# Kernel tuning notes

Measured on AMD Instinct MI355X. Metric: run time of the kernel, lower is better.

## Reference

```python
import jax, jax.numpy as jnp
import numpy as np

B, D, C, P = 1024, 768, 150, 64  # batch, in_feats, num_labels, proj2 dim
POS_M, NEG_M = 0.7, 1.4


def setup_inputs() -> dict:
    key = jax.random.key(0)
    ks = jax.random.split(key, 8)
    return {
        "x": jax.random.normal(ks[0], (B, D), jnp.float32),
        "lb": jax.random.randint(ks[1], (B,), 0, C + 1),
        "mem": jax.random.normal(ks[2], (C, D), jnp.float32),
        "fc_w": jax.random.normal(ks[3], (2 * D, 2 * D), jnp.float32) * 0.02,
        "fc_b": jnp.zeros((2 * D,), jnp.float32),
        "p1_w": jax.random.normal(ks[4], (1, 2 * D), jnp.float32) * 0.02,
        "p1_b": jnp.zeros((1,), jnp.float32),
        "p2_w": jax.random.normal(ks[5], (P, 2 * D), jnp.float32) * 0.02,
        "p2_b": jnp.zeros((P,), jnp.float32),
    }


def reference(x, lb, mem, fc_w, fc_b, p1_w, p1_b, p2_w, p2_b):
    d = x.shape[1]
    # cat([a, b], 1) @ fc_w.T == a @ Wx.T + b @ Wm.T  (exact split of the linear)
    Wx, Wm = fc_w[:, :d], fc_w[:, d:]
    xh = x @ Wx.T + fc_b                                # [B, 2D]

    # --- get_logit ---
    seen_h = jax.nn.relu(xh[:, None, :] + mem @ Wm.T)   # [B, C, 2D]
    seen = jnp.einsum('bce,e->bc', seen_h, p1_w[0]) + p1_b[0]   # [B, C]
    uh = jax.nn.relu(xh)                                # cat([x, zeros]) path
    unseen = uh @ p1_w.T + p1_b                         # [B, 1]
    logits = jnp.concatenate([seen, unseen], axis=1)    # [B, C+1]

    # --- masked log-softmax losses (pos_adapte) ---
    labels = jax.nn.one_hot(lb, C + 1, dtype=jnp.float32)
    th = jnp.zeros_like(labels).at[:, -1].set(1.0)
    labels = labels.at[:, -1].set(0.0)
    p_mask = labels + th
    n_mask = 1.0 - labels
    BIG = 1e30
    loss1 = -(jax.nn.log_softmax(logits - (1.0 - p_mask) * BIG, -1) * labels).sum(1)
    loss2 = -(jax.nn.log_softmax(logits - (1.0 - n_mask) * BIG, -1) * th).sum(1)
    loss_cls = (loss1 + loss2).mean()

    # --- metric loss on unseen embedding ---
    u = uh @ p2_w.T + p2_b                              # [B, 64]
    u = u / jnp.maximum(jnp.linalg.norm(u, axis=1, keepdims=True), 1e-12)
    sq_n = (u * u).sum(1)
    sq = sq_n[:, None] + sq_n[None, :] - 2.0 * (u @ u.T)
    err = sq <= 0.0
    dist = jnp.sqrt(jnp.clip(sq, 1e-16, None)) * (~err).astype(u.dtype)
    same = lb[:, None] == lb[None, :]
    eye = jnp.eye(dist.shape[0], dtype=bool)
    pos = (same & ~eye).astype(dist.dtype)
    neg = (~same).astype(dist.dtype)
    pos_l = (jax.nn.relu(dist - POS_M) * pos).sum() / jnp.maximum(pos.sum(), 1.0)
    neg_l = (jax.nn.relu(NEG_M - dist) * neg).sum() / jnp.maximum(neg.sum(), 1.0)

    return loss_cls + pos_l + neg_l
```

## Files before the change

kernel.cpp:

```cpp
#include <hip/hip_runtime.h>
#include <math.h>

#define B_    1024
#define D_    768
#define C_    150
#define P_    64
#define TWOD  1536
#define NCLS  151
#define CPAD  256

#define ECHUNKS 16
#define ECHUNK  96

#define ASTR  40
#define USTRU 120
#define USTR  72

#define OFF_MH      0
#define OFF_XH      (OFF_MH + (C_ * TWOD) / 2)
#define OFF_PARTIAL (OFF_XH + (B_ * TWOD) / 2)
#define OFF_UHF     (OFF_PARTIAL + ECHUNKS * B_ * CPAD)
#define OFF_SQN     (OFF_UHF + (B_ * P_) / 2)
#define OFF_CLS     (OFF_SQN + B_)
#define OFF_PAIR    (OFF_CLS + B_)
#define OFF_XBF     (OFF_PAIR + 1024)
#define OFF_MEMBF   (OFF_XBF + (B_ * D_) / 2)
#define OFF_WBF     (OFF_MEMBF + (C_ * D_) / 2)
#define OFF_P2H     (OFF_WBF + (TWOD * TWOD) / 2)
#define OFF_P1H     (OFF_P2H + (P_ * TWOD) / 2)

typedef __bf16    bfx8   __attribute__((ext_vector_type(8)));
typedef _Float16  fp16x8 __attribute__((ext_vector_type(8)));
typedef _Float16  h2v    __attribute__((ext_vector_type(2)));
typedef float     f32x4  __attribute__((ext_vector_type(4)));

__device__ inline ushort f2bf(float f) {
    union { float f; unsigned u; } c; c.f = f;
    unsigned r = c.u + 0x7fffu + ((c.u >> 16) & 1u);
    return (ushort)(r >> 16);
}
__device__ inline ushort f2h(float f) {
    _Float16 h = (_Float16)f;
    return __builtin_bit_cast(ushort, h);
}
__device__ inline unsigned addrelu2(unsigned a, unsigned m) {
    h2v s = __builtin_bit_cast(h2v, a) + __builtin_bit_cast(h2v, m);
    h2v z = {(_Float16)0.f, (_Float16)0.f};
    s = __builtin_elementwise_max(s, z);
    return __builtin_bit_cast(unsigned, s);
}
__device__ inline unsigned relu2(unsigned a) {
    h2v s = __builtin_bit_cast(h2v, a);
    h2v z = {(_Float16)0.f, (_Float16)0.f};
    s = __builtin_elementwise_max(s, z);
    return __builtin_bit_cast(unsigned, s);
}
__device__ inline float dot2acc(unsigned a, unsigned b, float c) {
    return __builtin_amdgcn_fdot2(__builtin_bit_cast(h2v, a),
                                  __builtin_bit_cast(h2v, b), c, false);
}

#define X4   (B_ * D_ / 4)
#define MEM4 (C_ * D_ / 4)
#define W4   (TWOD * TWOD / 4)
#define P24  (P_ * TWOD / 4)
#define P14  (TWOD / 4)
#define TOT4 (X4 + MEM4 + W4 + P24 + P14)

__global__ __launch_bounds__(256) void prep_cvt(
    const float* __restrict__ x, const float* __restrict__ mem,
    const float* __restrict__ w, const float* __restrict__ p2w,
    const float* __restrict__ p1w,
    ushort* __restrict__ xb, ushort* __restrict__ memb,
    ushort* __restrict__ wb, ushort* __restrict__ p2h,
    ushort* __restrict__ p1h)
{
    int i = blockIdx.x * 256 + threadIdx.x;
    if (i >= TOT4) return;
    const float* src; ushort* dst; int off; bool bf;
    if (i < X4)                        { src = x;   dst = xb;   off = i; bf = true; }
    else if (i < X4 + MEM4)            { src = mem; dst = memb; off = i - X4; bf = true; }
    else if (i < X4 + MEM4 + W4)       { src = w;   dst = wb;   off = i - X4 - MEM4; bf = true; }
    else if (i < X4 + MEM4 + W4 + P24) { src = p2w; dst = p2h;  off = i - X4 - MEM4 - W4; bf = false; }
    else                               { src = p1w; dst = p1h;  off = i - X4 - MEM4 - W4 - P24; bf = false; }
    float4 v = ((const float4*)src)[off];
    ushort4 o;
    if (bf) { o.x = f2bf(v.x); o.y = f2bf(v.y); o.z = f2bf(v.z); o.w = f2bf(v.w); }
    else    { o.x = f2h(v.x);  o.y = f2h(v.y);  o.z = f2h(v.z);  o.w = f2h(v.w); }
    ((ushort4*)dst)[off] = o;
}

__global__ __launch_bounds__(256) void gemm_all(
    const ushort* __restrict__ xbf, const ushort* __restrict__ membf,
    const ushort* __restrict__ wbf, const float* __restrict__ fc_b,
    ushort* __restrict__ xh, ushort* __restrict__ mh)
{
    __shared__ ushort As[64 * ASTR];
    __shared__ ushort Bs[128 * ASTR];
    const int id = blockIdx.x;
    const int t  = threadIdx.x;

    const ushort* A; ushort* Out; int M, m0, n0, koff; bool xblk;
    if (id < 192) {
        xblk = true;  A = xbf;  Out = xh; M = B_;
        m0 = (id & 15) * 64; n0 = (id >> 4) * 128; koff = 0;
    } else {
        int q = id - 192;
        xblk = false; A = membf; Out = mh; M = C_;
        m0 = (q % 3) * 64; n0 = (q / 3) * 128; koff = D_;
    }

    const int wave = t >> 6, lane = t & 63;
    const int wm = (wave & 1) * 32, wn = (wave >> 1) * 64;
    const int fm = lane & 15, quad = lane >> 4;

    const int row_a = t >> 2, qa = (t & 3) * 8;
    const int ar = min(m0 + row_a, M - 1);
    const ushort* Arow = A + (size_t)ar * D_ + qa;
    const ushort* Brow = wbf + (size_t)(n0 + row_a) * TWOD + koff + qa;

    f32x4 acc[2][4];
#pragma unroll
    for (int j = 0; j < 4; ++j) {
        float bv = xblk ? fc_b[n0 + wn + j * 16 + fm] : 0.f;
#pragma unroll
        for (int i = 0; i < 2; ++i)
            acc[i][j] = (f32x4){bv, bv, bv, bv};
    }

    uint4 pa  = *(const uint4*)(Arow);
    uint4 pb0 = *(const uint4*)(Brow);
    uint4 pb1 = *(const uint4*)(Brow + 64 * TWOD);

    for (int k0 = 0; k0 < D_; k0 += 32) {
        __syncthreads();
        *(uint4*)&As[row_a * ASTR + qa] = pa;
        *(uint4*)&Bs[row_a * ASTR + qa] = pb0;
        *(uint4*)&Bs[(64 + row_a) * ASTR + qa] = pb1;
        __syncthreads();
        if (k0 + 32 < D_) {
            pa  = *(const uint4*)(Arow + k0 + 32);
            pb0 = *(const uint4*)(Brow + k0 + 32);
            pb1 = *(const uint4*)(Brow + 64 * TWOD + k0 + 32);
        }
        bfx8 af[2], bf[4];
#pragma unroll
        for (int i = 0; i < 2; ++i)
            af[i] = *(const bfx8*)&As[(wm + i * 16 + fm) * ASTR + quad * 8];
#pragma unroll
        for (int j = 0; j < 4; ++j)
            bf[j] = *(const bfx8*)&Bs[(wn + j * 16 + fm) * ASTR + quad * 8];
#pragma unroll
        for (int i = 0; i < 2; ++i)
#pragma unroll
            for (int j = 0; j < 4; ++j)
                acc[i][j] = __builtin_amdgcn_mfma_f32_16x16x32_bf16(
                    af[i], bf[j], acc[i][j], 0, 0, 0);
    }

#pragma unroll
    for (int i = 0; i < 2; ++i)
#pragma unroll
        for (int j = 0; j < 4; ++j)
#pragma unroll
            for (int r = 0; r < 4; ++r) {
                int row = m0 + wm + i * 16 + quad * 4 + r;
                int col = n0 + wn + j * 16 + fm;
                if (row < M) Out[(size_t)row * TWOD + col] = f2h(acc[i][j][r]);
            }
}

__global__ __launch_bounds__(256) void fused_tile(
    const ushort* __restrict__ xh, const ushort* __restrict__ mh,
    const ushort* __restrict__ p1h, const ushort* __restrict__ p2h,
    float* __restrict__ partial)
{
    __shared__ __align__(16) char smem[46080];
    const int t  = threadIdx.x;
    const int b0 = blockIdx.x * 128;
    const int z  = blockIdx.z;
    const int e0 = z * ECHUNK;

    if (blockIdx.y == 3) {
        ushort* Au = (ushort*)smem;
        ushort* Wu = (ushort*)(smem + 30720);
        const int wave = t >> 6, lane = t & 63;
        const int fm = lane & 15, quad = lane >> 4;

        {
            const int row = t >> 1, kh = (t & 1) * 48;
            const ushort* src = xh + (size_t)(b0 + row) * TWOD + e0 + kh;
            uint4 v[6];
#pragma unroll
            for (int i = 0; i < 6; ++i) v[i] = *(const uint4*)&src[i * 8];
#pragma unroll
            for (int i = 0; i < 6; ++i) {
                v[i].x = relu2(v[i].x); v[i].y = relu2(v[i].y);
                v[i].z = relu2(v[i].z); v[i].w = relu2(v[i].w);
                *(uint4*)&Au[row * USTRU + kh + i * 8] = v[i];
            }
        }
        {
            const int row = t >> 2, ks = (t & 3) * 24;
            const ushort* pw = p2h + (size_t)row * TWOD + e0 + ks;
#pragma unroll
            for (int i = 0; i < 3; ++i)
                *(uint4*)&Wu[row * USTRU + ks + i * 8] = *(const uint4*)&pw[i * 8];
        }
        __syncthreads();

        f32x4 uacc[2][4];
#pragma unroll
        for (int i = 0; i < 2; ++i)
#pragma unroll
            for (int j = 0; j < 4; ++j) uacc[i][j] = (f32x4){0.f, 0.f, 0.f, 0.f};
#pragma unroll
        for (int k0 = 0; k0 < ECHUNK; k0 += 32) {
            fp16x8 af[2], bf[4];
#pragma unroll
            for (int i = 0; i < 2; ++i)
                af[i] = *(const fp16x8*)&Au[(wave * 32 + i * 16 + fm) * USTRU + k0 + quad * 8];
#pragma unroll
            for (int j = 0; j < 4; ++j)
                bf[j] = *(const fp16x8*)&Wu[(j * 16 + fm) * USTRU + k0 + quad * 8];
#pragma unroll
            for (int i = 0; i < 2; ++i)
#pragma unroll
                for (int j = 0; j < 4; ++j)
                    uacc[i][j] = __builtin_amdgcn_mfma_f32_16x16x32_f16(
                        af[i], bf[j], uacc[i][j], 0, 0, 0);
        }
#pragma unroll
        for (int i = 0; i < 2; ++i)
#pragma unroll
            for (int j = 0; j < 4; ++j)
#pragma unroll
                for (int r = 0; r < 4; ++r) {
                    int row = b0 + wave * 32 + i * 16 + quad * 4 + r;
                    partial[((size_t)z * B_ + row) * CPAD + 192 + j * 16 + fm] =
                        uacc[i][j][r];
                }
        return;
    }

    unsigned* xT = (unsigned*)smem;
    unsigned* mT = (unsigned*)(smem + 24576);
    unsigned* wT = (unsigned*)(smem + 36864);
    const int c0 = blockIdx.y * 64;
    const int tm = t & 15, tn = t >> 4;

    {
        const int row = t >> 1, ph = (t & 1) * 48;
        const ushort* src = xh + (size_t)(b0 + row) * TWOD + e0 + ph;
        uint4 v[6];
#pragma unroll
        for (int i = 0; i < 6; ++i) v[i] = *(const uint4*)&src[i * 8];
#pragma unroll
        for (int i = 0; i < 6; ++i) {
            const int ep = (t & 1) * 24 + i * 4;
            xT[(ep + 0) * 128 + row] = v[i].x;
            xT[(ep + 1) * 128 + row] = v[i].y;
            xT[(ep + 2) * 128 + row] = v[i].z;
            xT[(ep + 3) * 128 + row] = v[i].w;
        }
    }
    {
        const int col = t & 63, seg = t >> 6;
        const int gc  = c0 + col;
        uint4 v[3];
        if (gc < C_) {
            const ushort* src = mh + (size_t)gc * TWOD + e0 + seg * 24;
#pragma unroll
            for (int i = 0; i < 3; ++i) v[i] = *(const uint4*)&src[i * 8];
        } else {
#pragma unroll
            for (int i = 0; i < 3; ++i) v[i] = make_uint4(0, 0, 0, 0);
        }
#pragma unroll
        for (int i = 0; i < 3; ++i) {
            const int ep = seg * 12 + i * 4;
            mT[(ep + 0) * 64 + col] = v[i].x;
            mT[(ep + 1) * 64 + col] = v[i].y;
            mT[(ep + 2) * 64 + col] = v[i].z;
            mT[(ep + 3) * 64 + col] = v[i].w;
        }
    }
    if (t < 12) {
        uint4 v = *(const uint4*)&p1h[e0 + t * 8];
        wT[t * 4 + 0] = v.x; wT[t * 4 + 1] = v.y;
        wT[t * 4 + 2] = v.z; wT[t * 4 + 3] = v.w;
    }
    __syncthreads();

    float acc[8][4] = {};
#pragma unroll 4
    for (int ep = 0; ep < 48; ++ep) {
        uint4 a0 = *(const uint4*)&xT[ep * 128 + tm * 8];
        uint4 a1 = *(const uint4*)&xT[ep * 128 + tm * 8 + 4];
        uint4 mj = *(const uint4*)&mT[ep * 64 + tn * 4];
        const unsigned wv = wT[ep];
        const unsigned aa[8] = {a0.x, a0.y, a0.z, a0.w, a1.x, a1.y, a1.z, a1.w};
        const unsigned mm[4] = {mj.x, mj.y, mj.z, mj.w};
#pragma unroll
        for (int i = 0; i < 8; ++i)
#pragma unroll
            for (int j = 0; j < 4; ++j)
                acc[i][j] = dot2acc(addrelu2(aa[i], mm[j]), wv, acc[i][j]);
    }

#pragma unroll
    for (int i = 0; i < 8; ++i) {
        const int gb = b0 + tm * 8 + i;
        float4 v = make_float4(acc[i][0], acc[i][1], acc[i][2], acc[i][3]);
        *(float4*)&partial[((size_t)z * B_ + gb) * CPAD + c0 + tn * 4] = v;
    }
}

__global__ __launch_bounds__(256) void reduce_row(
    const float* __restrict__ partial,
    const float* __restrict__ p1b, const float* __restrict__ p2b,
    const int* __restrict__ lb,
    ushort* __restrict__ uhf, float* __restrict__ sqn,
    float* __restrict__ clsbuf)
{
    const int b = blockIdx.x, t = threadIdx.x;
    float v = 0.f;
#pragma unroll
    for (int z = 0; z < ECHUNKS; ++z)
        v += partial[((size_t)z * B_ + b) * CPAD + t];
    if (t < NCLS)       v += p1b[0];
    else if (t >= 192)  v += p2b[t - 192];

    __shared__ float sval[256];
    sval[t] = v;
    __syncthreads();

    if (t < 64) {
        float uv = sval[192 + t];
        float s = uv * uv;
#pragma unroll
        for (int off = 32; off; off >>= 1) s += __shfl_xor(s, off);
        float inv = 1.f / fmaxf(sqrtf(s), 1e-12f);
        uhf[(size_t)b * P_ + t] = f2h(uv * inv);
        if (t == 0) sqn[b] = s * inv * inv;

        const int l = lb[b];
        float mx = -1e30f;
        for (int j = t; j < NCLS; j += 64)
            if (!(j == l && l < C_)) mx = fmaxf(mx, sval[j]);
#pragma unroll
        for (int off = 32; off; off >>= 1) mx = fmaxf(mx, __shfl_xor(mx, off));
        float se = 0.f;
        for (int j = t; j < NCLS; j += 64)
            if (!(j == l && l < C_)) se += expf(sval[j] - mx);
#pragma unroll
        for (int off = 32; off; off >>= 1) se += __shfl_xor(se, off);

        if (t == 0) {
            float l150  = sval[C_];
            float loss2 = mx + logf(se) - l150;
            float loss1 = 0.f;
            if (l < C_) {
                float a  = sval[l];
                float m2 = fmaxf(a, l150);
                loss1 = m2 - a + logf(expf(a - m2) + expf(l150 - m2));
            }
            clsbuf[b] = loss1 + loss2;
        }
    }
}

__global__ __launch_bounds__(256) void pair_loss(
    const ushort* __restrict__ uhf, const float* __restrict__ sqn,
    const int* __restrict__ lb, float* __restrict__ pairpart)
{
    __shared__ ushort ui_s[64 * USTR];
    __shared__ ushort uj_s[64 * USTR];
    __shared__ float sni[64], snj[64];
    __shared__ int   li[64],  lj[64];
    __shared__ float red[4][4];

    const int t  = threadIdx.x;
    const int i0 = blockIdx.x * 64, j0 = blockIdx.y * 64;

    for (int idx = t; idx < 512; idx += 256) {
        int row = idx >> 3, ch = (idx & 7) * 8;
        *(uint4*)&ui_s[row * USTR + ch] =
            *(const uint4*)&uhf[(size_t)(i0 + row) * P_ + ch];
        *(uint4*)&uj_s[row * USTR + ch] =
            *(const uint4*)&uhf[(size_t)(j0 + row) * P_ + ch];
    }
    if (t < 64)       { sni[t] = sqn[i0 + t]; li[t] = lb[i0 + t]; }
    else if (t < 128) { int q = t - 64; snj[q] = sqn[j0 + q]; lj[q] = lb[j0 + q]; }
    __syncthreads();

    const int wave = t >> 6, lane = t & 63;
    const int n = lane & 15, quad = lane >> 4;
    const int iw = wave * 16;

    const fp16x8 af0 = *(const fp16x8*)&ui_s[(iw + n) * USTR + quad * 8];
    const fp16x8 af1 = *(const fp16x8*)&ui_s[(iw + n) * USTR + quad * 8 + 32];

    f32x4 acc[4];
#pragma unroll
    for (int jt = 0; jt < 4; ++jt) {
        const fp16x8 bf0 = *(const fp16x8*)&uj_s[(jt * 16 + n) * USTR + quad * 8];
        const fp16x8 bf1 = *(const fp16x8*)&uj_s[(jt * 16 + n) * USTR + quad * 8 + 32];
        acc[jt] = __builtin_amdgcn_mfma_f32_16x16x32_f16(
            af0, bf0, (f32x4){0.f, 0.f, 0.f, 0.f}, 0, 0, 0);
        acc[jt] = __builtin_amdgcn_mfma_f32_16x16x32_f16(
            af1, bf1, acc[jt], 0, 0, 0);
    }

    float ps = 0.f, pc = 0.f, ns = 0.f, nc = 0.f;
#pragma unroll
    for (int jt = 0; jt < 4; ++jt)
#pragma unroll
        for (int r = 0; r < 4; ++r) {
            const int il = iw + quad * 4 + r;
            const int jl = jt * 16 + n;
            float sq = sni[il] + snj[jl] - 2.f * acc[jt][r];
            float dist = sq > 0.f ? sqrtf(fmaxf(sq, 1e-16f)) : 0.f;
            bool same = (li[il] == lj[jl]);
            if (same) {
                if (i0 + il != j0 + jl) { ps += fmaxf(dist - 0.7f, 0.f); pc += 1.f; }
            } else {
                ns += fmaxf(1.4f - dist, 0.f); nc += 1.f;
            }
        }

#pragma unroll
    for (int off = 32; off; off >>= 1) {
        ps += __shfl_xor(ps, off); pc += __shfl_xor(pc, off);
        ns += __shfl_xor(ns, off); nc += __shfl_xor(nc, off);
    }
    if (lane == 0) { red[0][wave] = ps; red[1][wave] = pc;
                     red[2][wave] = ns; red[3][wave] = nc; }
    __syncthreads();
    if (t == 0) {
        float4 v;
        v.x = red[0][0] + red[0][1] + red[0][2] + red[0][3];
        v.y = red[1][0] + red[1][1] + red[1][2] + red[1][3];
        v.z = red[2][0] + red[2][1] + red[2][2] + red[2][3];
        v.w = red[3][0] + red[3][1] + red[3][2] + red[3][3];
        *(float4*)&pairpart[(size_t)(blockIdx.y * 16 + blockIdx.x) * 4] = v;
    }
}

__global__ __launch_bounds__(256) void finalize(
    const float* __restrict__ clsbuf, const float* __restrict__ pairpart,
    float* __restrict__ out)
{
    __shared__ float red[5][4];
    const int t = threadIdx.x;
    float c = clsbuf[t] + clsbuf[t + 256] + clsbuf[t + 512] + clsbuf[t + 768];
    float4 pp = *(const float4*)&pairpart[(size_t)t * 4];
    float ps = pp.x, pc = pp.y, ns = pp.z, nc = pp.w;
#pragma unroll
    for (int off = 32; off; off >>= 1) {
        c  += __shfl_xor(c, off);
        ps += __shfl_xor(ps, off); pc += __shfl_xor(pc, off);
        ns += __shfl_xor(ns, off); nc += __shfl_xor(nc, off);
    }
    const int wave = t >> 6, lane = t & 63;
    if (lane == 0) { red[0][wave] = c; red[1][wave] = ps; red[2][wave] = pc;
                     red[3][wave] = ns; red[4][wave] = nc; }
    __syncthreads();
    if (t == 0) {
        float C = 0.f, PS = 0.f, PC = 0.f, NS = 0.f, NC = 0.f;
#pragma unroll
        for (int w = 0; w < 4; ++w) {
            C += red[0][w]; PS += red[1][w]; PC += red[2][w];
            NS += red[3][w]; NC += red[4][w];
        }
        out[0] = C / (float)B_ + PS / fmaxf(PC, 1.f) + NS / fmaxf(NC, 1.f);
    }
}

extern "C" void kernel_launch(void* const* d_in, const int* in_sizes, int n_in,
                              void* d_out, int out_size, void* d_ws, size_t ws_size,
                              hipStream_t stream)
{
    const float* x    = (const float*)d_in[0];
    const int*   lb   = (const int*)d_in[1];
    const float* mem  = (const float*)d_in[2];
    const float* fc_w = (const float*)d_in[3];
    const float* fc_b = (const float*)d_in[4];
    const float* p1w  = (const float*)d_in[5];
    const float* p1b  = (const float*)d_in[6];
    const float* p2w  = (const float*)d_in[7];
    const float* p2b  = (const float*)d_in[8];

    float* ws       = (float*)d_ws;
    ushort* mh      = (ushort*)(ws + OFF_MH);
    ushort* xh      = (ushort*)(ws + OFF_XH);
    float* partials = ws + OFF_PARTIAL;
    ushort* uhf     = (ushort*)(ws + OFF_UHF);
    float* sqn      = ws + OFF_SQN;
    float* clsbuf   = ws + OFF_CLS;
    float* pairpart = ws + OFF_PAIR;
    ushort* xbf     = (ushort*)(ws + OFF_XBF);
    ushort* membf   = (ushort*)(ws + OFF_MEMBF);
    ushort* wbf     = (ushort*)(ws + OFF_WBF);
    ushort* p2h     = (ushort*)(ws + OFF_P2H);
    ushort* p1h     = (ushort*)(ws + OFF_P1H);

    prep_cvt<<<(TOT4 + 255) / 256, 256, 0, stream>>>(x, mem, fc_w, p2w, p1w,
                                                     xbf, membf, wbf, p2h, p1h);
    gemm_all<<<228, 256, 0, stream>>>(xbf, membf, wbf, fc_b, xh, mh);
    fused_tile<<<dim3(8, 4, ECHUNKS), 256, 0, stream>>>(xh, mh, p1h, p2h,
                                                        partials);
    reduce_row<<<B_, 256, 0, stream>>>(partials, p1b, p2b, lb, uhf, sqn, clsbuf);
    pair_loss<<<dim3(16, 16), 256, 0, stream>>>(uhf, sqn, lb, pairpart);
    finalize<<<1, 256, 0, stream>>>(clsbuf, pairpart, (float*)d_out);
}
```

Measured before the change: 132.2 us.

## Merge six kernel launches into one cooperative persistent kernel with grid syncs

Replaces the sequence of prep, GEMM, fused tile, row reduce, pair loss and finalize kernels with a single cooperative kernel of 512 blocks. The stages are separated by grid-wide barriers. This removes per-launch overhead and the gaps between dependent kernels. In exchange, each stage is limited to 512 resident blocks, idle blocks wait at every barrier, and grid.sync itself has a cost.

New measurement: 403.9 us. +205.6%, slower.

```diff
diff --git a/kernel.cpp b/kernel.cpp
--- a/kernel.cpp
+++ b/kernel.cpp
@@ -1,5 +1,8 @@
 #include <hip/hip_runtime.h>
+#include <hip/hip_cooperative_groups.h>
 #include <math.h>
+
+namespace cg = cooperative_groups;
 
 #define B_    1024
 #define D_    768
@@ -67,413 +70,424 @@
 #define P14  (TWOD / 4)
 #define TOT4 (X4 + MEM4 + W4 + P24 + P14)
 
-__global__ __launch_bounds__(256) void prep_cvt(
-    const float* __restrict__ x, const float* __restrict__ mem,
-    const float* __restrict__ w, const float* __restrict__ p2w,
-    const float* __restrict__ p1w,
-    ushort* __restrict__ xb, ushort* __restrict__ memb,
-    ushort* __restrict__ wb, ushort* __restrict__ p2h,
-    ushort* __restrict__ p1h)
+#define GRID_ 512
+
+__global__ __launch_bounds__(256, 2) void mega(
+    const float* __restrict__ x, const int* __restrict__ lb,
+    const float* __restrict__ mem, const float* __restrict__ fcw,
+    const float* __restrict__ fcb, const float* __restrict__ p1w,
+    const float* __restrict__ p1b, const float* __restrict__ p2w,
+    const float* __restrict__ p2b, float* __restrict__ ws,
+    float* __restrict__ out)
 {
-    int i = blockIdx.x * 256 + threadIdx.x;
-    if (i >= TOT4) return;
-    const float* src; ushort* dst; int off; bool bf;
-    if (i < X4)                        { src = x;   dst = xb;   off = i; bf = true; }
-    else if (i < X4 + MEM4)            { src = mem; dst = memb; off = i - X4; bf = true; }
-    else if (i < X4 + MEM4 + W4)       { src = w;   dst = wb;   off = i - X4 - MEM4; bf = true; }
-    else if (i < X4 + MEM4 + W4 + P24) { src = p2w; dst = p2h;  off = i - X4 - MEM4 - W4; bf = false; }
-    else                               { src = p1w; dst = p1h;  off = i - X4 - MEM4 - W4 - P24; bf = false; }
-    float4 v = ((const float4*)src)[off];
-    ushort4 o;
-    if (bf) { o.x = f2bf(v.x); o.y = f2bf(v.y); o.z = f2bf(v.z); o.w = f2bf(v.w); }
-    else    { o.x = f2h(v.x);  o.y = f2h(v.y);  o.z = f2h(v.z);  o.w = f2h(v.w); }
-    ((ushort4*)dst)[off] = o;
-}
-
-__global__ __launch_bounds__(256) void gemm_all(
-    const ushort* __restrict__ xbf, const ushort* __restrict__ membf,
-    const ushort* __restrict__ wbf, const float* __restrict__ fc_b,
-    ushort* __restrict__ xh, ushort* __restrict__ mh)
-{
-    __shared__ ushort As[64 * ASTR];
-    __shared__ ushort Bs[128 * ASTR];
+    __shared__ __align__(16) char smem[46080];
+    cg::grid_group grid = cg::this_grid();
     const int id = blockIdx.x;
     const int t  = threadIdx.x;
 
-    const ushort* A; ushort* Out; int M, m0, n0, koff; bool xblk;
-    if (id < 192) {
-        xblk = true;  A = xbf;  Out = xh; M = B_;
-        m0 = (id & 15) * 64; n0 = (id >> 4) * 128; koff = 0;
-    } else {
-        int q = id - 192;
-        xblk = false; A = membf; Out = mh; M = C_;
-        m0 = (q % 3) * 64; n0 = (q / 3) * 128; koff = D_;
+    ushort* mh       = (ushort*)(ws + OFF_MH);
+    ushort* xh       = (ushort*)(ws + OFF_XH);
+    float*  partial  = ws + OFF_PARTIAL;
+    ushort* uhf      = (ushort*)(ws + OFF_UHF);
+    float*  sqn      = ws + OFF_SQN;
+    float*  clsbuf   = ws + OFF_CLS;
+    float*  pairpart = ws + OFF_PAIR;
+    ushort* xbf      = (ushort*)(ws + OFF_XBF);
+    ushort* membf    = (ushort*)(ws + OFF_MEMBF);
+    ushort* wbf      = (ushort*)(ws + OFF_WBF);
+    ushort* p2h      = (ushort*)(ws + OFF_P2H);
+    ushort* p1h      = (ushort*)(ws + OFF_P1H);
+
+    for (int i = id * 256 + t; i < TOT4; i += GRID_ * 256) {
+        const float* src; ushort* dst; int off; bool bf;
+        if (i < X4)                        { src = x;   dst = xbf;   off = i; bf = true; }
+        else if (i < X4 + MEM4)            { src = mem; dst = membf; off = i - X4; bf = true; }
+        else if (i < X4 + MEM4 + W4)       { src = fcw; dst = wbf;   off = i - X4 - MEM4; bf = true; }
+        else if (i < X4 + MEM4 + W4 + P24) { src = p2w; dst = p2h;   off = i - X4 - MEM4 - W4; bf = false; }
+        else                               { src = p1w; dst = p1h;   off = i - X4 - MEM4 - W4 - P24; bf = false; }
+        float4 v = ((const float4*)src)[off];
+        ushort4 o;
+        if (bf) { o.x = f2bf(v.x); o.y = f2bf(v.y); o.z = f2bf(v.z); o.w = f2bf(v.w); }
+        else    { o.x = f2h(v.x);  o.y = f2h(v.y);  o.z = f2h(v.z);  o.w = f2h(v.w); }
+        ((ushort4*)dst)[off] = o;
     }
 
-    const int wave = t >> 6, lane = t & 63;
-    const int wm = (wave & 1) * 32, wn = (wave >> 1) * 64;
-    const int fm = lane & 15, quad = lane >> 4;
-
-    const int row_a = t >> 2, qa = (t & 3) * 8;
-    const int ar = min(m0 + row_a, M - 1);
-    const ushort* Arow = A + (size_t)ar * D_ + qa;
-    const ushort* Brow = wbf + (size_t)(n0 + row_a) * TWOD + koff + qa;
-
-    f32x4 acc[2][4];
-#pragma unroll
-    for (int j = 0; j < 4; ++j) {
-        float bv = xblk ? fc_b[n0 + wn + j * 16 + fm] : 0.f;
+    grid.sync();
+
+    if (id < 228) {
+        ushort* As = (ushort*)smem;
+        ushort* Bs = (ushort*)(smem + 5120);
+
+        const ushort* A; ushort* Out; int M, m0, n0, koff; bool xblk;
+        if (id < 192) {
+            xblk = true;  A = xbf;   Out = xh; M = B_;
+            m0 = (id & 15) * 64; n0 = (id >> 4) * 128; koff = 0;
+        } else {
+            int q = id - 192;
+            xblk = false; A = membf; Out = mh; M = C_;
+            m0 = (q % 3) * 64; n0 = (q / 3) * 128; koff = D_;
+        }
+
+        const int wave = t >> 6, lane = t & 63;
+        const int wm = (wave & 1) * 32, wn = (wave >> 1) * 64;
+        const int fm = lane & 15, quad = lane >> 4;
+
+        const int row_a = t >> 2, qa = (t & 3) * 8;
+        const int ar = min(m0 + row_a, M - 1);
+        const ushort* Arow = A + (size_t)ar * D_ + qa;
+        const ushort* Brow = wbf + (size_t)(n0 + row_a) * TWOD + koff + qa;
+
+        f32x4 acc[2][4];
+#pragma unroll
+        for (int j = 0; j < 4; ++j) {
+            float bv = xblk ? fcb[n0 + wn + j * 16 + fm] : 0.f;
+#pragma unroll
+            for (int i = 0; i < 2; ++i)
+                acc[i][j] = (f32x4){bv, bv, bv, bv};
+        }
+
+        uint4 pa  = *(const uint4*)(Arow);
+        uint4 pb0 = *(const uint4*)(Brow);
+        uint4 pb1 = *(const uint4*)(Brow + 64 * TWOD);
+
+        for (int k0 = 0; k0 < D_; k0 += 32) {
+            __syncthreads();
+            *(uint4*)&As[row_a * ASTR + qa] = pa;
+            *(uint4*)&Bs[row_a * ASTR + qa] = pb0;
+            *(uint4*)&Bs[(64 + row_a) * ASTR + qa] = pb1;
+            __syncthreads();
+            if (k0 + 32 < D_) {
+                pa  = *(const uint4*)(Arow + k0 + 32);
+                pb0 = *(const uint4*)(Brow + k0 + 32);
+                pb1 = *(const uint4*)(Brow + 64 * TWOD + k0 + 32);
+            }
+            bfx8 af[2], bf[4];
+#pragma unroll
+            for (int i = 0; i < 2; ++i)
+                af[i] = *(const bfx8*)&As[(wm + i * 16 + fm) * ASTR + quad * 8];
+#pragma unroll
+            for (int j = 0; j < 4; ++j)
+                bf[j] = *(const bfx8*)&Bs[(wn + j * 16 + fm) * ASTR + quad * 8];
+#pragma unroll
+            for (int i = 0; i < 2; ++i)
+#pragma unroll
+                for (int j = 0; j < 4; ++j)
+                    acc[i][j] = __builtin_amdgcn_mfma_f32_16x16x32_bf16(
+                        af[i], bf[j], acc[i][j], 0, 0, 0);
+        }
+
 #pragma unroll
         for (int i = 0; i < 2; ++i)
-            acc[i][j] = (f32x4){bv, bv, bv, bv};
+#pragma unroll
+            for (int j = 0; j < 4; ++j)
+#pragma unroll
+                for (int r = 0; r < 4; ++r) {
+                    int row = m0 + wm + i * 16 + quad * 4 + r;
+                    int col = n0 + wn + j * 16 + fm;
+                    if (row < M) Out[(size_t)row * TWOD + col] = f2h(acc[i][j][r]);
+                }
     }
 
-    uint4 pa  = *(const uint4*)(Arow);
-    uint4 pb0 = *(const uint4*)(Brow);
-    uint4 pb1 = *(const uint4*)(Brow + 64 * TWOD);
-
-    for (int k0 = 0; k0 < D_; k0 += 32) {
+    grid.sync();
+
+    {
+        const int bx = id & 7, yy = (id >> 3) & 3, z = id >> 5;
+        const int b0 = bx * 128;
+        const int e0 = z * ECHUNK;
+
+        if (yy == 3) {
+            ushort* Au = (ushort*)smem;
+            ushort* Wu = (ushort*)(smem + 30720);
+            const int wave = t >> 6, lane = t & 63;
+            const int fm = lane & 15, quad = lane >> 4;
+
+            {
+                const int row = t >> 1, kh = (t & 1) * 48;
+                const ushort* src = xh + (size_t)(b0 + row) * TWOD + e0 + kh;
+                uint4 v[6];
+#pragma unroll
+                for (int i = 0; i < 6; ++i) v[i] = *(const uint4*)&src[i * 8];
+#pragma unroll
+                for (int i = 0; i < 6; ++i) {
+                    v[i].x = relu2(v[i].x); v[i].y = relu2(v[i].y);
+                    v[i].z = relu2(v[i].z); v[i].w = relu2(v[i].w);
+                    *(uint4*)&Au[row * USTRU + kh + i * 8] = v[i];
+                }
+            }
+            {
+                const int row = t >> 2, ks = (t & 3) * 24;
+                const ushort* pw = p2h + (size_t)row * TWOD + e0 + ks;
+#pragma unroll
+                for (int i = 0; i < 3; ++i)
+                    *(uint4*)&Wu[row * USTRU + ks + i * 8] = *(const uint4*)&pw[i * 8];
+            }
+            __syncthreads();
+
+            f32x4 uacc[2][4];
+#pragma unroll
+            for (int i = 0; i < 2; ++i)
+#pragma unroll
+                for (int j = 0; j < 4; ++j) uacc[i][j] = (f32x4){0.f, 0.f, 0.f, 0.f};
+#pragma unroll
+            for (int k0 = 0; k0 < ECHUNK; k0 += 32) {
+                fp16x8 af[2], bf[4];
+#pragma unroll
+                for (int i = 0; i < 2; ++i)
+                    af[i] = *(const fp16x8*)&Au[(wave * 32 + i * 16 + fm) * USTRU + k0 + quad * 8];
+#pragma unroll
+                for (int j = 0; j < 4; ++j)
+                    bf[j] = *(const fp16x8*)&Wu[(j * 16 + fm) * USTRU + k0 + quad * 8];
+#pragma unroll
+                for (int i = 0; i < 2; ++i)
+#pragma unroll
+                    for (int j = 0; j < 4; ++j)
+                        uacc[i][j] = __builtin_amdgcn_mfma_f32_16x16x32_f16(
+                            af[i], bf[j], uacc[i][j], 0, 0, 0);
+            }
+#pragma unroll
+            for (int i = 0; i < 2; ++i)
+#pragma unroll
+                for (int j = 0; j < 4; ++j)
+#pragma unroll
+                    for (int r = 0; r < 4; ++r) {
+                        int row = b0 + wave * 32 + i * 16 + quad * 4 + r;
+                        partial[((size_t)z * B_ + row) * CPAD + 192 + j * 16 + fm] =
+                            uacc[i][j][r];
+                    }
+        } else {
+            unsigned* xT = (unsigned*)smem;
+            unsigned* mT = (unsigned*)(smem + 24576);
+            unsigned* wT = (unsigned*)(smem + 36864);
+            const int c0 = yy * 64;
+            const int tm = t & 15, tn = t >> 4;
+
+            {
+                const int row = t >> 1, ph = (t & 1) * 48;
+                const ushort* src = xh + (size_t)(b0 + row) * TWOD + e0 + ph;
+                uint4 v[6];
+#pragma unroll
+                for (int i = 0; i < 6; ++i) v[i] = *(const uint4*)&src[i * 8];
+#pragma unroll
+                for (int i = 0; i < 6; ++i) {
+                    const int ep = (t & 1) * 24 + i * 4;
+                    xT[(ep + 0) * 128 + row] = v[i].x;
+                    xT[(ep + 1) * 128 + row] = v[i].y;
+                    xT[(ep + 2) * 128 + row] = v[i].z;
+                    xT[(ep + 3) * 128 + row] = v[i].w;
+                }
+            }
+            {
+                const int col = t & 63, seg = t >> 6;
+                const int gc  = c0 + col;
+                uint4 v[3];
+                if (gc < C_) {
+                    const ushort* src = mh + (size_t)gc * TWOD + e0 + seg * 24;
+#pragma unroll
+                    for (int i = 0; i < 3; ++i) v[i] = *(const uint4*)&src[i * 8];
+                } else {
+#pragma unroll
+                    for (int i = 0; i < 3; ++i) v[i] = make_uint4(0, 0, 0, 0);
+                }
+#pragma unroll
+                for (int i = 0; i < 3; ++i) {
+                    const int ep = seg * 12 + i * 4;
+                    mT[(ep + 0) * 64 + col] = v[i].x;
+                    mT[(ep + 1) * 64 + col] = v[i].y;
+                    mT[(ep + 2) * 64 + col] = v[i].z;
+                    mT[(ep + 3) * 64 + col] = v[i].w;
+                }
+            }
+            if (t < 12) {
+                uint4 v = *(const uint4*)&p1h[e0 + t * 8];
+                wT[t * 4 + 0] = v.x; wT[t * 4 + 1] = v.y;
+                wT[t * 4 + 2] = v.z; wT[t * 4 + 3] = v.w;
+            }
+            __syncthreads();
+
+            float acc[8][4] = {};
+#pragma unroll 4
+            for (int ep = 0; ep < 48; ++ep) {
+                uint4 a0 = *(const uint4*)&xT[ep * 128 + tm * 8];
+                uint4 a1 = *(const uint4*)&xT[ep * 128 + tm * 8 + 4];
+                uint4 mj = *(const uint4*)&mT[ep * 64 + tn * 4];
+                const unsigned wv = wT[ep];
+                const unsigned aa[8] = {a0.x, a0.y, a0.z, a0.w,
+                                        a1.x, a1.y, a1.z, a1.w};
+                const unsigned mm[4] = {mj.x, mj.y, mj.z, mj.w};
+#pragma unroll
+                for (int i = 0; i < 8; ++i)
+#pragma unroll
+                    for (int j = 0; j < 4; ++j)
+                        acc[i][j] = dot2acc(addrelu2(aa[i], mm[j]), wv, acc[i][j]);
+            }
+
+#pragma unroll
+            for (int i = 0; i < 8; ++i) {
+                const int gb = b0 + tm * 8 + i;
+                float4 v = make_float4(acc[i][0], acc[i][1], acc[i][2], acc[i][3]);
+                *(float4*)&partial[((size_t)z * B_ + gb) * CPAD + c0 + tn * 4] = v;
+            }
+        }
+    }
+
+    grid.sync();
+
+    {
+        float* sval = (float*)smem;
+        for (int rr = 0; rr < 2; ++rr) {
+            const int b = id * 2 + rr;
+            float v = 0.f;
+#pragma unroll
+            for (int z = 0; z < ECHUNKS; ++z)
+                v += partial[((size_t)z * B_ + b) * CPAD + t];
+            if (t < NCLS)       v += p1b[0];
+            else if (t >= 192)  v += p2b[t - 192];
+
+            __syncthreads();
+            sval[t] = v;
+            __syncthreads();
+
+            if (t < 64) {
+                float uv = sval[192 + t];
+                float s = uv * uv;
+#pragma unroll
+                for (int off = 32; off; off >>= 1) s += __shfl_xor(s, off);
+                float inv = 1.f / fmaxf(sqrtf(s), 1e-12f);
+                uhf[(size_t)b * P_ + t] = f2h(uv * inv);
+                if (t == 0) sqn[b] = s * inv * inv;
+
+                const int l = lb[b];
+                float mx = -1e30f;
+                for (int j = t; j < NCLS; j += 64)
+                    if (!(j == l && l < C_)) mx = fmaxf(mx, sval[j]);
+#pragma unroll
+                for (int off = 32; off; off >>= 1) mx = fmaxf(mx, __shfl_xor(mx, off));
+                float se = 0.f;
+                for (int j = t; j < NCLS; j += 64)
+                    if (!(j == l && l < C_)) se += expf(sval[j] - mx);
+#pragma unroll
+                for (int off = 32; off; off >>= 1) se += __shfl_xor(se, off);
+
+                if (t == 0) {
+                    float l150  = sval[C_];
+                    float loss2 = mx + logf(se) - l150;
+                    float loss1 = 0.f;
+                    if (l < C_) {
+                        float a  = sval[l];
+                        float m2 = fmaxf(a, l150);
+                        loss1 = m2 - a + logf(expf(a - m2) + expf(l150 - m2));
+                    }
+                    clsbuf[b] = loss1 + loss2;
+                }
+            }
+        }
+    }
+
+    grid.sync();
+
+    if (id < 256) {
+        ushort* ui_s = (ushort*)smem;
+        ushort* uj_s = (ushort*)(smem + 9216);
+        float*  sni  = (float*)(smem + 18432);
+        float*  snj  = (float*)(smem + 18688);
+        int*    li   = (int*)(smem + 18944);
+        int*    lj   = (int*)(smem + 19200);
+        float*  red  = (float*)(smem + 19456);
+
+        const int i0 = (id & 15) * 64, j0 = (id >> 4) * 64;
+
+        for (int idx = t; idx < 512; idx += 256) {
+            int row = idx >> 3, ch = (idx & 7) * 8;
+            *(uint4*)&ui_s[row * USTR + ch] =
+                *(const uint4*)&uhf[(size_t)(i0 + row) * P_ + ch];
+            *(uint4*)&uj_s[row * USTR + ch] =
+                *(const uint4*)&uhf[(size_t)(j0 + row) * P_ + ch];
+        }
+        if (t < 64)       { sni[t] = sqn[i0 + t]; li[t] = lb[i0 + t]; }
+        else if (t < 128) { int q = t - 64; snj[q] = sqn[j0 + q]; lj[q] = lb[j0 + q]; }
         __syncthreads();
-        *(uint4*)&As[row_a * ASTR + qa] = pa;
-        *(uint4*)&Bs[row_a * ASTR + qa] = pb0;
-        *(uint4*)&Bs[(64 + row_a) * ASTR + qa] = pb1;
+
+        const int wave = t >> 6, lane = t & 63;
+        const int n = lane & 15, quad = lane >> 4;
+        const int iw = wave * 16;
+
+        const fp16x8 af0 = *(const fp16x8*)&ui_s[(iw + n) * USTR + quad * 8];
+        const fp16x8 af1 = *(const fp16x8*)&ui_s[(iw + n) * USTR + quad * 8 + 32];
+
+        f32x4 acc[4];
+#pragma unroll
+        for (int jt = 0; jt < 4; ++jt) {
+            const fp16x8 bf0 = *(const fp16x8*)&uj_s[(jt * 16 + n) * USTR + quad * 8];
+            const fp16x8 bf1 = *(const fp16x8*)&uj_s[(jt * 16 + n) * USTR + quad * 8 + 32];
+            acc[jt] = __builtin_amdgcn_mfma_f32_16x16x32_f16(
+                af0, bf0, (f32x4){0.f, 0.f, 0.f, 0.f}, 0, 0, 0);
+            acc[jt] = __builtin_amdgcn_mfma_f32_16x16x32_f16(
+                af1, bf1, acc[jt], 0, 0, 0);
+        }
+
+        float ps = 0.f, pc = 0.f, ns = 0.f, nc = 0.f;
+#pragma unroll
+        for (int jt = 0; jt < 4; ++jt)
+#pragma unroll
+            for (int r = 0; r < 4; ++r) {
+                const int il = iw + quad * 4 + r;
+                const int jl = jt * 16 + n;
+                float sq = sni[il] + snj[jl] - 2.f * acc[jt][r];
+                float dist = sq > 0.f ? sqrtf(fmaxf(sq, 1e-16f)) : 0.f;
+                bool same = (li[il] == lj[jl]);
+                if (same) {
+                    if (i0 + il != j0 + jl) { ps += fmaxf(dist - 0.7f, 0.f); pc += 1.f; }
+                } else {
+                    ns += fmaxf(1.4f - dist, 0.f); nc += 1.f;
+                }
+            }
+
+#pragma unroll
+        for (int off = 32; off; off >>= 1) {
+            ps += __shfl_xor(ps, off); pc += __shfl_xor(pc, off);
+            ns += __shfl_xor(ns, off); nc += __shfl_xor(nc, off);
+        }
+        if (lane == 0) { red[0 * 4 + wave] = ps; red[1 * 4 + wave] = pc;
+                         red[2 * 4 + wave] = ns; red[3 * 4 + wave] = nc; }
         __syncthreads();
-        if (k0 + 32 < D_) {
-            pa  = *(const uint4*)(Arow + k0 + 32);
-            pb0 = *(const uint4*)(Brow + k0 + 32);
-            pb1 = *(const uint4*)(Brow + 64 * TWOD + k0 + 32);
-        }
-        bfx8 af[2], bf[4];
-#pragma unroll
-        for (int i = 0; i < 2; ++i)
-            af[i] = *(const bfx8*)&As[(wm + i * 16 + fm) * ASTR + quad * 8];
-#pragma unroll
-        for (int j = 0; j < 4; ++j)
-            bf[j] = *(const bfx8*)&Bs[(wn + j * 16 + fm) * ASTR + quad * 8];
-#pragma unroll
-        for (int i = 0; i < 2; ++i)
-#pragma unroll
-            for (int j = 0; j < 4; ++j)
-                acc[i][j] = __builtin_amdgcn_mfma_f32_16x16x32_bf16(
-                    af[i], bf[j], acc[i][j], 0, 0, 0);
+        if (t == 0) {
+            float4 v;
+            v.x = red[0] + red[1] + red[2] + red[3];
+            v.y = red[4] + red[5] + red[6] + red[7];
+            v.z = red[8] + red[9] + red[10] + red[11];
+            v.w = red[12] + red[13] + red[14] + red[15];
+            *(float4*)&pairpart[(size_t)id * 4] = v;
+        }
     }
 
-#pragma unroll
-    for (int i = 0; i < 2; ++i)
-#pragma unroll
-        for (int j = 0; j < 4; ++j)
-#pragma unroll
-            for (int r = 0; r < 4; ++r) {
-                int row = m0 + wm + i * 16 + quad * 4 + r;
-                int col = n0 + wn + j * 16 + fm;
-                if (row < M) Out[(size_t)row * TWOD + col] = f2h(acc[i][j][r]);
-            }
-}
-
-__global__ __launch_bounds__(256) void fused_tile(
-    const ushort* __restrict__ xh, const ushort* __restrict__ mh,
-    const ushort* __restrict__ p1h, const ushort* __restrict__ p2h,
-    float* __restrict__ partial)
-{
-    __shared__ __align__(16) char smem[46080];
-    const int t  = threadIdx.x;
-    const int b0 = blockIdx.x * 128;
-    const int z  = blockIdx.z;
-    const int e0 = z * ECHUNK;
-
-    if (blockIdx.y == 3) {
-        ushort* Au = (ushort*)smem;
-        ushort* Wu = (ushort*)(smem + 30720);
+    grid.sync();
+
+    if (id == 0) {
+        float* red = (float*)smem;
+        float c = clsbuf[t] + clsbuf[t + 256] + clsbuf[t + 512] + clsbuf[t + 768];
+        float4 pp = *(const float4*)&pairpart[(size_t)t * 4];
+        float ps = pp.x, pc = pp.y, ns = pp.z, nc = pp.w;
+#pragma unroll
+        for (int off = 32; off; off >>= 1) {
+            c  += __shfl_xor(c, off);
+            ps += __shfl_xor(ps, off); pc += __shfl_xor(pc, off);
+            ns += __shfl_xor(ns, off); nc += __shfl_xor(nc, off);
+        }
         const int wave = t >> 6, lane = t & 63;
-        const int fm = lane & 15, quad = lane >> 4;
-
-        {
-            const int row = t >> 1, kh = (t & 1) * 48;
-            const ushort* src = xh + (size_t)(b0 + row) * TWOD + e0 + kh;
-            uint4 v[6];
-#pragma unroll
-            for (int i = 0; i < 6; ++i) v[i] = *(const uint4*)&src[i * 8];
-#pragma unroll
-            for (int i = 0; i < 6; ++i) {
-                v[i].x = relu2(v[i].x); v[i].y = relu2(v[i].y);
-                v[i].z = relu2(v[i].z); v[i].w = relu2(v[i].w);
-                *(uint4*)&Au[row * USTRU + kh + i * 8] = v[i];
-            }
-        }
-        {
-            const int row = t >> 2, ks = (t & 3) * 24;
-            const ushort* pw = p2h + (size_t)row * TWOD + e0 + ks;
-#pragma unroll
-            for (int i = 0; i < 3; ++i)
-                *(uint4*)&Wu[row * USTRU + ks + i * 8] = *(const uint4*)&pw[i * 8];
-        }
         __syncthreads();
-
-        f32x4 uacc[2][4];
-#pragma unroll
-        for (int i = 0; i < 2; ++i)
-#pragma unroll
-            for (int j = 0; j < 4; ++j) uacc[i][j] = (f32x4){0.f, 0.f, 0.f, 0.f};
-#pragma unroll
-        for (int k0 = 0; k0 < ECHUNK; k0 += 32) {
-            fp16x8 af[2], bf[4];
-#pragma unroll
-            for (int i = 0; i < 2; ++i)
-                af[i] = *(const fp16x8*)&Au[(wave * 32 + i * 16 + fm) * USTRU + k0 + quad * 8];
-#pragma unroll
-            for (int j = 0; j < 4; ++j)
-                bf[j] = *(const fp16x8*)&Wu[(j * 16 + fm) * USTRU + k0 + quad * 8];
-#pragma unroll
-            for (int i = 0; i < 2; ++i)
-#pragma unroll
-                for (int j = 0; j < 4; ++j)
-                    uacc[i][j] = __builtin_amdgcn_mfma_f32_16x16x32_f16(
-                        af[i], bf[j], uacc[i][j], 0, 0, 0);
-        }
-#pragma unroll
-        for (int i = 0; i < 2; ++i)
-#pragma unroll
-            for (int j = 0; j < 4; ++j)
-#pragma unroll
-                for (int r = 0; r < 4; ++r) {
-                    int row = b0 + wave * 32 + i * 16 + quad * 4 + r;
-                    partial[((size_t)z * B_ + row) * CPAD + 192 + j * 16 + fm] =
-                        uacc[i][j][r];
-                }
-        return;
-    }
-
-    unsigned* xT = (unsigned*)smem;
-    unsigned* mT = (unsigned*)(smem + 24576);
-    unsigned* wT = (unsigned*)(smem + 36864);
-    const int c0 = blockIdx.y * 64;
-    const int tm = t & 15, tn = t >> 4;
-
-    {
-        const int row = t >> 1, ph = (t & 1) * 48;
-        const ushort* src = xh + (size_t)(b0 + row) * TWOD + e0 + ph;
-        uint4 v[6];
-#pragma unroll
-        for (int i = 0; i < 6; ++i) v[i] = *(const uint4*)&src[i * 8];
-#pragma unroll
-        for (int i = 0; i < 6; ++i) {
-            const int ep = (t & 1) * 24 + i * 4;
-            xT[(ep + 0) * 128 + row] = v[i].x;
-            xT[(ep + 1) * 128 + row] = v[i].y;
-            xT[(ep + 2) * 128 + row] = v[i].z;
-            xT[(ep + 3) * 128 + row] = v[i].w;
-        }
-    }
-    {
-        const int col = t & 63, seg = t >> 6;
-        const int gc  = c0 + col;
-        uint4 v[3];
-        if (gc < C_) {
-            const ushort* src = mh + (size_t)gc * TWOD + e0 + seg * 24;
-#pragma unroll
-            for (int i = 0; i < 3; ++i) v[i] = *(const uint4*)&src[i * 8];
-        } else {
-#pragma unroll
-            for (int i = 0; i < 3; ++i) v[i] = make_uint4(0, 0, 0, 0);
-        }
-#pragma unroll
-        for (int i = 0; i < 3; ++i) {
-            const int ep = seg * 12 + i * 4;
-            mT[(ep + 0) * 64 + col] = v[i].x;
-            mT[(ep + 1) * 64 + col] = v[i].y;
-            mT[(ep + 2) * 64 + col] = v[i].z;
-            mT[(ep + 3) * 64 + col] = v[i].w;
-        }
-    }
-    if (t < 12) {
-        uint4 v = *(const uint4*)&p1h[e0 + t * 8];
-        wT[t * 4 + 0] = v.x; wT[t * 4 + 1] = v.y;
-        wT[t * 4 + 2] = v.z; wT[t * 4 + 3] = v.w;
-    }
-    __syncthreads();
-
-    float acc[8][4] = {};
-#pragma unroll 4
-    for (int ep = 0; ep < 48; ++ep) {
-        uint4 a0 = *(const uint4*)&xT[ep * 128 + tm * 8];
-        uint4 a1 = *(const uint4*)&xT[ep * 128 + tm * 8 + 4];
-        uint4 mj = *(const uint4*)&mT[ep * 64 + tn * 4];
-        const unsigned wv = wT[ep];
-        const unsigned aa[8] = {a0.x, a0.y, a0.z, a0.w, a1.x, a1.y, a1.z, a1.w};
-        const unsigned mm[4] = {mj.x, mj.y, mj.z, mj.w};
-#pragma unroll
-        for (int i = 0; i < 8; ++i)
-#pragma unroll
-            for (int j = 0; j < 4; ++j)
-                acc[i][j] = dot2acc(addrelu2(aa[i], mm[j]), wv, acc[i][j]);
-    }
-
-#pragma unroll
-    for (int i = 0; i < 8; ++i) {
-        const int gb = b0 + tm * 8 + i;
-        float4 v = make_float4(acc[i][0], acc[i][1], acc[i][2], acc[i][3]);
-        *(float4*)&partial[((size_t)z * B_ + gb) * CPAD + c0 + tn * 4] = v;
-    }
-}
-
-__global__ __launch_bounds__(256) void reduce_row(
-    const float* __restrict__ partial,
-    const float* __restrict__ p1b, const float* __restrict__ p2b,
-    const int* __restrict__ lb,
-    ushort* __restrict__ uhf, float* __restrict__ sqn,
-    float* __restrict__ clsbuf)
-{
-    const int b = blockIdx.x, t = threadIdx.x;
-    float v = 0.f;
-#pragma unroll
-    for (int z = 0; z < ECHUNKS; ++z)
-        v += partial[((size_t)z * B_ + b) * CPAD + t];
-    if (t < NCLS)       v += p1b[0];
-    else if (t >= 192)  v += p2b[t - 192];
-
-    __shared__ float sval[256];
-    sval[t] = v;
-    __syncthreads();
-
-    if (t < 64) {
-        float uv = sval[192 + t];
-        float s = uv * uv;
-#pragma unroll
-        for (int off = 32; off; off >>= 1) s += __shfl_xor(s, off);
-        float inv = 1.f / fmaxf(sqrtf(s), 1e-12f);
-        uhf[(size_t)b * P_ + t] = f2h(uv * inv);
-        if (t == 0) sqn[b] = s * inv * inv;
-
-        const int l = lb[b];
-        float mx = -1e30f;
-        for (int j = t; j < NCLS; j += 64)
-            if (!(j == l && l < C_)) mx = fmaxf(mx, sval[j]);
-#pragma unroll
-        for (int off = 32; off; off >>= 1) mx = fmaxf(mx, __shfl_xor(mx, off));
-        float se = 0.f;
-        for (int j = t; j < NCLS; j += 64)
-            if (!(j == l && l < C_)) se += expf(sval[j] - mx);
-#pragma unroll
-        for (int off = 32; off; off >>= 1) se += __shfl_xor(se, off);
-
+        if (lane == 0) { red[0 * 4 + wave] = c; red[1 * 4 + wave] = ps;
+                         red[2 * 4 + wave] = pc; red[3 * 4 + wave] = ns;
+                         red[4 * 4 + wave] = nc; }
+        __syncthreads();
         if (t == 0) {
-            float l150  = sval[C_];
-            float loss2 = mx + logf(se) - l150;
-            float loss1 = 0.f;
-            if (l < C_) {
-                float a  = sval[l];
-                float m2 = fmaxf(a, l150);
-                loss1 = m2 - a + logf(expf(a - m2) + expf(l150 - m2));
-            }
-            clsbuf[b] = loss1 + loss2;
-        }
-    }
-}
-
-__global__ __launch_bounds__(256) void pair_loss(
-    const ushort* __restrict__ uhf, const float* __restrict__ sqn,
-    const int* __restrict__ lb, float* __restrict__ pairpart)
-{
-    __shared__ ushort ui_s[64 * USTR];
-    __shared__ ushort uj_s[64 * USTR];
-    __shared__ float sni[64], snj[64];
-    __shared__ int   li[64],  lj[64];
-    __shared__ float red[4][4];
-
-    const int t  = threadIdx.x;
-    const int i0 = blockIdx.x * 64, j0 = blockIdx.y * 64;
-
-    for (int idx = t; idx < 512; idx += 256) {
-        int row = idx >> 3, ch = (idx & 7) * 8;
-        *(uint4*)&ui_s[row * USTR + ch] =
-            *(const uint4*)&uhf[(size_t)(i0 + row) * P_ + ch];
-        *(uint4*)&uj_s[row * USTR + ch] =
-            *(const uint4*)&uhf[(size_t)(j0 + row) * P_ + ch];
-    }
-    if (t < 64)       { sni[t] = sqn[i0 + t]; li[t] = lb[i0 + t]; }
-    else if (t < 128) { int q = t - 64; snj[q] = sqn[j0 + q]; lj[q] = lb[j0 + q]; }
-    __syncthreads();
-
-    const int wave = t >> 6, lane = t & 63;
-    const int n = lane & 15, quad = lane >> 4;
-    const int iw = wave * 16;
-
-    const fp16x8 af0 = *(const fp16x8*)&ui_s[(iw + n) * USTR + quad * 8];
-    const fp16x8 af1 = *(const fp16x8*)&ui_s[(iw + n) * USTR + quad * 8 + 32];
-
-    f32x4 acc[4];
-#pragma unroll
-    for (int jt = 0; jt < 4; ++jt) {
-        const fp16x8 bf0 = *(const fp16x8*)&uj_s[(jt * 16 + n) * USTR + quad * 8];
-        const fp16x8 bf1 = *(const fp16x8*)&uj_s[(jt * 16 + n) * USTR + quad * 8 + 32];
-        acc[jt] = __builtin_amdgcn_mfma_f32_16x16x32_f16(
-            af0, bf0, (f32x4){0.f, 0.f, 0.f, 0.f}, 0, 0, 0);
-        acc[jt] = __builtin_amdgcn_mfma_f32_16x16x32_f16(
-            af1, bf1, acc[jt], 0, 0, 0);
-    }
-
-    float ps = 0.f, pc = 0.f, ns = 0.f, nc = 0.f;
-#pragma unroll
-    for (int jt = 0; jt < 4; ++jt)
-#pragma unroll
-        for (int r = 0; r < 4; ++r) {
-            const int il = iw + quad * 4 + r;
-            const int jl = jt * 16 + n;
-            float sq = sni[il] + snj[jl] - 2.f * acc[jt][r];
-            float dist = sq > 0.f ? sqrtf(fmaxf(sq, 1e-16f)) : 0.f;
-            bool same = (li[il] == lj[jl]);
-            if (same) {
-                if (i0 + il != j0 + jl) { ps += fmaxf(dist - 0.7f, 0.f); pc += 1.f; }
-            } else {
-                ns += fmaxf(1.4f - dist, 0.f); nc += 1.f;
-            }
-        }
-
-#pragma unroll
-    for (int off = 32; off; off >>= 1) {
-        ps += __shfl_xor(ps, off); pc += __shfl_xor(pc, off);
-        ns += __shfl_xor(ns, off); nc += __shfl_xor(nc, off);
-    }
-    if (lane == 0) { red[0][wave] = ps; red[1][wave] = pc;
-                     red[2][wave] = ns; red[3][wave] = nc; }
-    __syncthreads();
-    if (t == 0) {
-        float4 v;
-        v.x = red[0][0] + red[0][1] + red[0][2] + red[0][3];
-        v.y = red[1][0] + red[1][1] + red[1][2] + red[1][3];
-        v.z = red[2][0] + red[2][1] + red[2][2] + red[2][3];
-        v.w = red[3][0] + red[3][1] + red[3][2] + red[3][3];
-        *(float4*)&pairpart[(size_t)(blockIdx.y * 16 + blockIdx.x) * 4] = v;
-    }
-}
-
-__global__ __launch_bounds__(256) void finalize(
-    const float* __restrict__ clsbuf, const float* __restrict__ pairpart,
-    float* __restrict__ out)
-{
-    __shared__ float red[5][4];
-    const int t = threadIdx.x;
-    float c = clsbuf[t] + clsbuf[t + 256] + clsbuf[t + 512] + clsbuf[t + 768];
-    float4 pp = *(const float4*)&pairpart[(size_t)t * 4];
-    float ps = pp.x, pc = pp.y, ns = pp.z, nc = pp.w;
-#pragma unroll
-    for (int off = 32; off; off >>= 1) {
-        c  += __shfl_xor(c, off);
-        ps += __shfl_xor(ps, off); pc += __shfl_xor(pc, off);
-        ns += __shfl_xor(ns, off); nc += __shfl_xor(nc, off);
-    }
-    const int wave = t >> 6, lane = t & 63;
-    if (lane == 0) { red[0][wave] = c; red[1][wave] = ps; red[2][wave] = pc;
-                     red[3][wave] = ns; red[4][wave] = nc; }
-    __syncthreads();
-    if (t == 0) {
-        float C = 0.f, PS = 0.f, PC = 0.f, NS = 0.f, NC = 0.f;
-#pragma unroll
-        for (int w = 0; w < 4; ++w) {
-            C += red[0][w]; PS += red[1][w]; PC += red[2][w];
-            NS += red[3][w]; NC += red[4][w];
-        }
-        out[0] = C / (float)B_ + PS / fmaxf(PC, 1.f) + NS / fmaxf(NC, 1.f);
+            float C = 0.f, PS = 0.f, PC = 0.f, NS = 0.f, NC = 0.f;
+#pragma unroll
+            for (int w = 0; w < 4; ++w) {
+                C += red[0 * 4 + w]; PS += red[1 * 4 + w]; PC += red[2 * 4 + w];
+                NS += red[3 * 4 + w]; NC += red[4 * 4 + w];
+            }
+            out[0] = C / (float)B_ + PS / fmaxf(PC, 1.f) + NS / fmaxf(NC, 1.f);
+        }
     }
 }
 
@@ -490,27 +504,14 @@
     const float* p1b  = (const float*)d_in[6];
     const float* p2w  = (const float*)d_in[7];
     const float* p2b  = (const float*)d_in[8];
-
-    float* ws       = (float*)d_ws;
-    ushort* mh      = (ushort*)(ws + OFF_MH);
-    ushort* xh      = (ushort*)(ws + OFF_XH);
-    float* partials = ws + OFF_PARTIAL;
-    ushort* uhf     = (ushort*)(ws + OFF_UHF);
-    float* sqn      = ws + OFF_SQN;
-    float* clsbuf   = ws + OFF_CLS;
-    float* pairpart = ws + OFF_PAIR;
-    ushort* xbf     = (ushort*)(ws + OFF_XBF);
-    ushort* membf   = (ushort*)(ws + OFF_MEMBF);
-    ushort* wbf     = (ushort*)(ws + OFF_WBF);
-    ushort* p2h     = (ushort*)(ws + OFF_P2H);
-    ushort* p1h     = (ushort*)(ws + OFF_P1H);
-
-    prep_cvt<<<(TOT4 + 255) / 256, 256, 0, stream>>>(x, mem, fc_w, p2w, p1w,
-                                                     xbf, membf, wbf, p2h, p1h);
-    gemm_all<<<228, 256, 0, stream>>>(xbf, membf, wbf, fc_b, xh, mh);
-    fused_tile<<<dim3(8, 4, ECHUNKS), 256, 0, stream>>>(xh, mh, p1h, p2h,
-                                                        partials);
-    reduce_row<<<B_, 256, 0, stream>>>(partials, p1b, p2b, lb, uhf, sqn, clsbuf);
-    pair_loss<<<dim3(16, 16), 256, 0, stream>>>(uhf, sqn, lb, pairpart);
-    finalize<<<1, 256, 0, stream>>>(clsbuf, pairpart, (float*)d_out);
-}
+    float* ws  = (float*)d_ws;
+    float* out = (float*)d_out;
+
+    void* args[] = {
+        (void*)&x, (void*)&lb, (void*)&mem, (void*)&fc_w, (void*)&fc_b,
+        (void*)&p1w, (void*)&p1b, (void*)&p2w, (void*)&p2b,
+        (void*)&ws, (void*)&out
+    };
+    hipLaunchCooperativeKernel((void*)mega, dim3(GRID_), dim3(256),
+                               args, 0, stream);
+}
```
